# Kernel optimization log

Measured on AMD Instinct MI355X. Metric: run time of the kernel, lower is better.

## Reference

```python
import jax, jax.numpy as jnp
import numpy as np

B, N, NFEAT, NHID, NOUT, NMLP, NCLASS = 32, 1024, 128, 64, 64, 128, 2
ALPHA = 0.2  # leaky relu slope
NEG = -9e15


def setup_inputs() -> dict:
    key = jax.random.key(0)
    ks = jax.random.split(key, 12)
    x = jax.random.normal(ks[0], (B, N, NFEAT), dtype=jnp.float32)
    x_mask = (jax.random.uniform(ks[1], (B, N)) < 0.9).astype(jnp.float32)
    adj = (jax.random.uniform(ks[2], (B, N, N)) < 0.05).astype(jnp.float32)
    adj = jnp.maximum(adj, jnp.eye(N, dtype=jnp.float32)[None])  # self loops
    s = 0.02
    W0 = jax.random.normal(ks[3], (NFEAT, NHID), dtype=jnp.float32) * s
    a0 = jax.random.normal(ks[4], (2 * NHID, 1), dtype=jnp.float32) * s
    Wout = jax.random.normal(ks[5], (NHID, NOUT), dtype=jnp.float32) * s
    aout = jax.random.normal(ks[6], (2 * NOUT, 1), dtype=jnp.float32) * s
    W1 = jax.random.normal(ks[7], (NOUT, NMLP), dtype=jnp.float32) * s
    b1 = jnp.zeros((NMLP,), dtype=jnp.float32)
    W2 = jax.random.normal(ks[8], (NMLP, NCLASS), dtype=jnp.float32) * s
    b2 = jnp.zeros((NCLASS,), dtype=jnp.float32)
    return {"x": x, "x_mask": x_mask, "adj": adj, "W0": W0, "a0": a0,
            "Wout": Wout, "aout": aout, "W1": W1, "b1": b1, "W2": W2, "b2": b2}


def _gat_layer(h, adj, W, a):
    # h: [B,N,F_in], W: [F_in,F_out], a: [2*F_out,1]
    Wh = jnp.einsum('bnf,fh->bnh', h, W)                 # [B,N,F_out]
    d = W.shape[1]
    f1 = Wh @ a[:d]                                      # [B,N,1]
    f2 = Wh @ a[d:]                                      # [B,N,1]
    e = jax.nn.leaky_relu(f1 + jnp.swapaxes(f2, 1, 2), ALPHA)  # [B,N,N]
    e = jnp.where(adj > 0, e, NEG)
    attn = jax.nn.softmax(e, axis=-1)
    return jnp.einsum('bnm,bmh->bnh', attn, Wh)


def reference(x, x_mask, adj, W0, a0, Wout, aout, W1, b1, W2, b2):
    # Only head 0 reaches out_att in the original (zip truncation); dropout is
    # identity in eval mode.
    h = jax.nn.elu(_gat_layer(x, adj, W0, a0))           # concat=True -> elu
    h = jax.nn.elu(_gat_layer(h, adj, Wout, aout))       # F.elu applied outside
    m = x_mask[..., None]
    g = jnp.sum(h * m, axis=1) / jnp.maximum(jnp.sum(x_mask, axis=1, keepdims=True), 1.0)  # masked mean readout [B,NOUT]
    return jax.nn.relu(g @ W1 + b1) @ W2 + b2            # [B,NCLASS]
```

## Files before the change

kernel.cpp:

```cpp
#include <hip/hip_runtime.h>
#include <math.h>

#define BB 32
#define NN 1024
#define NFEAT 128
#define ALPHA 0.2f
#define MAXD 128

#define WH1_TILE_BLOCKS (BB * NN / 64)
#define BM_BLOCKS (BB * NN / 4)
#define ATTN_BLOCKS (BB * NN / 8)

template<int FIN>
__device__ __forceinline__ void wh_tile_body(
    const int blk, const int tid,
    const float* __restrict__ hin, const float* __restrict__ W,
    const float* __restrict__ a, float* __restrict__ Wh,
    float* __restrict__ f1, float* __restrict__ f2) {
  const int tx = tid & 15;
  const int ty = tid >> 4;
  const int row0 = blk * 64 + ty * 4;

  float4 acc[4];
#pragma unroll
  for (int i = 0; i < 4; ++i) acc[i] = make_float4(0.f, 0.f, 0.f, 0.f);

#pragma unroll 4
  for (int k = 0; k < FIN; k += 4) {
    float4 wv[4];
#pragma unroll
    for (int i = 0; i < 4; ++i)
      wv[i] = *reinterpret_cast<const float4*>(&W[(size_t)(k + i) * 64 + tx * 4]);
#pragma unroll
    for (int i = 0; i < 4; ++i) {
      const float4 xv = *reinterpret_cast<const float4*>(
          &hin[(size_t)(row0 + i) * FIN + k]);
      acc[i].x = fmaf(xv.x, wv[0].x, acc[i].x);
      acc[i].y = fmaf(xv.x, wv[0].y, acc[i].y);
      acc[i].z = fmaf(xv.x, wv[0].z, acc[i].z);
      acc[i].w = fmaf(xv.x, wv[0].w, acc[i].w);
      acc[i].x = fmaf(xv.y, wv[1].x, acc[i].x);
      acc[i].y = fmaf(xv.y, wv[1].y, acc[i].y);
      acc[i].z = fmaf(xv.y, wv[1].z, acc[i].z);
      acc[i].w = fmaf(xv.y, wv[1].w, acc[i].w);
      acc[i].x = fmaf(xv.z, wv[2].x, acc[i].x);
      acc[i].y = fmaf(xv.z, wv[2].y, acc[i].y);
      acc[i].z = fmaf(xv.z, wv[2].z, acc[i].z);
      acc[i].w = fmaf(xv.z, wv[2].w, acc[i].w);
      acc[i].x = fmaf(xv.w, wv[3].x, acc[i].x);
      acc[i].y = fmaf(xv.w, wv[3].y, acc[i].y);
      acc[i].z = fmaf(xv.w, wv[3].z, acc[i].z);
      acc[i].w = fmaf(xv.w, wv[3].w, acc[i].w);
    }
  }

  const float4 av1 = *reinterpret_cast<const float4*>(&a[tx * 4]);
  const float4 av2 = *reinterpret_cast<const float4*>(&a[64 + tx * 4]);
#pragma unroll
  for (int i = 0; i < 4; ++i) {
    const int row = row0 + i;
    *reinterpret_cast<float4*>(&Wh[(size_t)row * 64 + tx * 4]) = acc[i];
    float c1 = acc[i].x * av1.x + acc[i].y * av1.y + acc[i].z * av1.z + acc[i].w * av1.w;
    float c2 = acc[i].x * av2.x + acc[i].y * av2.y + acc[i].z * av2.z + acc[i].w * av2.w;
#pragma unroll
    for (int off = 8; off > 0; off >>= 1) {
      c1 += __shfl_xor(c1, off, 64);
      c2 += __shfl_xor(c2, off, 64);
    }
    if (tx == 0) { f1[row] = c1; f2[row] = c2; }
  }
}

__global__ __launch_bounds__(256) void wh1_kernel(
    const float* __restrict__ x, const float* __restrict__ W0,
    const float* __restrict__ a0, float* __restrict__ Wh,
    float* __restrict__ f1, float* __restrict__ f2) {
  wh_tile_body<NFEAT>(blockIdx.x, threadIdx.x, x, W0, a0, Wh, f1, f2);
}

__global__ __launch_bounds__(256) void bitmask_kernel(
    const float* __restrict__ adj, unsigned short* __restrict__ bm) {
  const int wv = threadIdx.x >> 6, lane = threadIdx.x & 63;
  const int row = blockIdx.x * 4 + wv;
  const float* ar = adj + (size_t)row * NN + lane * 16;
  const float4 a0 = *reinterpret_cast<const float4*>(ar);
  const float4 a1 = *reinterpret_cast<const float4*>(ar + 4);
  const float4 a2 = *reinterpret_cast<const float4*>(ar + 8);
  const float4 a3 = *reinterpret_cast<const float4*>(ar + 12);
  unsigned m = 0;
  m |= (a0.x > 0.f ? 1u : 0u);        m |= (a0.y > 0.f ? 2u : 0u);
  m |= (a0.z > 0.f ? 4u : 0u);        m |= (a0.w > 0.f ? 8u : 0u);
  m |= (a1.x > 0.f ? 16u : 0u);       m |= (a1.y > 0.f ? 32u : 0u);
  m |= (a1.z > 0.f ? 64u : 0u);       m |= (a1.w > 0.f ? 128u : 0u);
  m |= (a2.x > 0.f ? 256u : 0u);      m |= (a2.y > 0.f ? 512u : 0u);
  m |= (a2.z > 0.f ? 1024u : 0u);     m |= (a2.w > 0.f ? 2048u : 0u);
  m |= (a3.x > 0.f ? 4096u : 0u);     m |= (a3.y > 0.f ? 8192u : 0u);
  m |= (a3.z > 0.f ? 16384u : 0u);    m |= (a3.w > 0.f ? 32768u : 0u);
  bm[(size_t)row * 64 + lane] = (unsigned short)m;
}

__device__ __forceinline__ int bit_compact(
    const unsigned short* __restrict__ bmrow, unsigned short* msh,
    const int lane) {
  unsigned w = bmrow[lane];
  const int myc = __popc(w);
  int pre = myc;
#pragma unroll
  for (int off = 1; off < 64; off <<= 1) {
    const int v = __shfl_up(pre, off, 64);
    if (lane >= off) pre += v;
  }
  const int total = __shfl(pre, 63, 64);
  int base = pre - myc;
  while (w) {
    const int b = __ffs(w) - 1;
    if (base < MAXD) msh[base] = (unsigned short)(lane * 16 + b);
    w &= w - 1;
    ++base;
  }
  return total < MAXD ? total : MAXD;
}

__device__ __forceinline__ void gather4(
    const float* ps0, const unsigned short* ms0,
    const float* ps1, const unsigned short* ms1,
    const int bound, const float* __restrict__ Whb,
    const int slot, const int fq, float4& outA, float4& outB) {
  float4 accA = make_float4(0.f, 0.f, 0.f, 0.f);
  float4 accB = make_float4(0.f, 0.f, 0.f, 0.f);
  const float* WhF = Whb + fq * 4;
  for (int k = 0; k < bound; k += 4) {
    const int ia = ms0[k + slot];
    const int ib = ms1[k + slot];
    const float pa = ps0[k + slot];
    const float pb = ps1[k + slot];
    const float4 wa = *reinterpret_cast<const float4*>(&WhF[(size_t)ia * 64]);
    const float4 wb = *reinterpret_cast<const float4*>(&WhF[(size_t)ib * 64]);
    accA.x = fmaf(pa, wa.x, accA.x);
    accA.y = fmaf(pa, wa.y, accA.y);
    accA.z = fmaf(pa, wa.z, accA.z);
    accA.w = fmaf(pa, wa.w, accA.w);
    accB.x = fmaf(pb, wb.x, accB.x);
    accB.y = fmaf(pb, wb.y, accB.y);
    accB.z = fmaf(pb, wb.z, accB.z);
    accB.w = fmaf(pb, wb.w, accB.w);
  }
#pragma unroll
  for (int off = 16; off <= 32; off <<= 1) {
    accA.x += __shfl_xor(accA.x, off, 64);
    accA.y += __shfl_xor(accA.y, off, 64);
    accA.z += __shfl_xor(accA.z, off, 64);
    accA.w += __shfl_xor(accA.w, off, 64);
    accB.x += __shfl_xor(accB.x, off, 64);
    accB.y += __shfl_xor(accB.y, off, 64);
    accB.z += __shfl_xor(accB.z, off, 64);
    accB.w += __shfl_xor(accB.w, off, 64);
  }
  outA = accA;
  outB = accB;
}

__device__ __forceinline__ float4 elu4(const float4 v) {
  return make_float4(v.x > 0.f ? v.x : expm1f(v.x),
                     v.y > 0.f ? v.y : expm1f(v.y),
                     v.z > 0.f ? v.z : expm1f(v.z),
                     v.w > 0.f ? v.w : expm1f(v.w));
}

__global__ __launch_bounds__(256) void attn1_kernel(
    const unsigned short* __restrict__ bm,
    const float* __restrict__ f1, const float* __restrict__ f2,
    const float* __restrict__ Wh,
    const float* __restrict__ Wnext, const float* __restrict__ anext,
    float* __restrict__ WhOut, float* __restrict__ f1o,
    float* __restrict__ f2o) {
  __shared__ __align__(16) float ps[4][2][MAXD];
  __shared__ __align__(16) unsigned short msh[4][2][MAXD];
  __shared__ __align__(16) float h1s[4][2][64];
  const int wv = threadIdx.x >> 6, lane = threadIdx.x & 63;
  const int slot = lane >> 4, fq = lane & 15;
  const int j = blockIdx.x;
  const int batch = (j & 7) + 8 * (j >> 10);
  const int cp = (j >> 3) & 127;
  const int row0 = (batch * 256 + 2 * cp) * 4 + wv;

  msh[wv][0][lane] = 0;  msh[wv][0][64 + lane] = 0;
  msh[wv][1][lane] = 0;  msh[wv][1][64 + lane] = 0;
  const int count0 = bit_compact(bm + (size_t)row0 * 64, msh[wv][0], lane);
  const int count1 = bit_compact(bm + (size_t)(row0 + 4) * 64, msh[wv][1], lane);

  const float f1v0 = f1[row0];
  const float f1v1 = f1[row0 + 4];
  const float* f2b = f2 + (size_t)batch * NN;
#pragma unroll
  for (int rr = 0; rr < 2; ++rr) {
    const int cntr = rr == 0 ? count0 : count1;
    const float f1n = rr == 0 ? f1v0 : f1v1;
    const int m0 = msh[wv][rr][lane];
    const int m1 = msh[wv][rr][64 + lane];
    const bool on0 = lane < cntr, on1 = 64 + lane < cntr;
    const float v0 = f1n + f2b[m0];
    const float v1 = f1n + f2b[m1];
    float e0v = on0 ? (v0 > 0.f ? v0 : ALPHA * v0) : -3e38f;
    float e1v = on1 ? (v1 > 0.f ? v1 : ALPHA * v1) : -3e38f;
    float lmax = fmaxf(e0v, e1v);
#pragma unroll
    for (int off = 32; off > 0; off >>= 1) lmax = fmaxf(lmax, __shfl_xor(lmax, off, 64));
    const float p0 = on0 ? __expf(e0v - lmax) : 0.f;
    const float p1 = on1 ? __expf(e1v - lmax) : 0.f;
    float ls = p0 + p1;
#pragma unroll
    for (int off = 32; off > 0; off >>= 1) ls += __shfl_xor(ls, off, 64);
    const float inv = 1.f / ls;
    ps[wv][rr][lane] = p0 * inv;
    ps[wv][rr][64 + lane] = p1 * inv;
  }

  const int cmax = count0 > count1 ? count0 : count1;
  const int bound = (cmax + 3) & ~3;
  const float* Whb = Wh + (size_t)batch * (NN * 64);
  float4 accA, accB;
  gather4(ps[wv][0], msh[wv][0], ps[wv][1], msh[wv][1], bound, Whb,
          slot, fq, accA, accB);
  if (slot == 0) {
    *reinterpret_cast<float4*>(&h1s[wv][0][fq * 4]) = elu4(accA);
    *reinterpret_cast<float4*>(&h1s[wv][1][fq * 4]) = elu4(accB);
  }

  float s0 = 0.f, s1 = 0.f;
#pragma unroll 8
  for (int f = 0; f < 64; ++f) {
    const float w = Wnext[f * 64 + lane];
    s0 = fmaf(h1s[wv][0][f], w, s0);
    s1 = fmaf(h1s[wv][1][f], w, s1);
  }
  WhOut[(size_t)row0 * 64 + lane] = s0;
  WhOut[(size_t)(row0 + 4) * 64 + lane] = s1;
  const float a1v = anext[lane], a2v = anext[64 + lane];
  float c10 = s0 * a1v, c20 = s0 * a2v;
  float c11 = s1 * a1v, c21 = s1 * a2v;
#pragma unroll
  for (int off = 32; off > 0; off >>= 1) {
    c10 += __shfl_xor(c10, off, 64);
    c20 += __shfl_xor(c20, off, 64);
    c11 += __shfl_xor(c11, off, 64);
    c21 += __shfl_xor(c21, off, 64);
  }
  if (lane == 0) {
    f1o[row0] = c10;  f2o[row0] = c20;
    f1o[row0 + 4] = c11;  f2o[row0 + 4] = c21;
  }
}

__global__ __launch_bounds__(256) void attn2_kernel(
    const unsigned short* __restrict__ bm,
    const float* __restrict__ f1, const float* __restrict__ f2,
    const float* __restrict__ Wh, const float* __restrict__ mask,
    float* __restrict__ part2) {
  __shared__ __align__(16) float ps[4][2][MAXD];
  __shared__ __align__(16) unsigned short msh[4][2][MAXD];
  __shared__ __align__(16) float agg[4][2][64];
  const int wv = threadIdx.x >> 6, lane = threadIdx.x & 63;
  const int slot = lane >> 4, fq = lane & 15;
  const int j = blockIdx.x;
  const int batch = (j & 7) + 8 * (j >> 10);
  const int cp = (j >> 3) & 127;
  const int row0 = (batch * 256 + 2 * cp) * 4 + wv;

  msh[wv][0][lane] = 0;  msh[wv][0][64 + lane] = 0;
  msh[wv][1][lane] = 0;  msh[wv][1][64 + lane] = 0;
  const int count0 = bit_compact(bm + (size_t)row0 * 64, msh[wv][0], lane);
  const int count1 = bit_compact(bm + (size_t)(row0 + 4) * 64, msh[wv][1], lane);

  const float* f2b = f2 + (size_t)batch * NN;
  const float f1v[2] = { f1[row0], f1[row0 + 4] };
#pragma unroll
  for (int rr = 0; rr < 2; ++rr) {
    const int cntr = rr == 0 ? count0 : count1;
    const int m0 = msh[wv][rr][lane];
    const int m1 = msh[wv][rr][64 + lane];
    const bool on0 = lane < cntr, on1 = 64 + lane < cntr;
    const float v0 = f1v[rr] + f2b[m0];
    const float v1 = f1v[rr] + f2b[m1];
    float e0v = on0 ? (v0 > 0.f ? v0 : ALPHA * v0) : -3e38f;
    float e1v = on1 ? (v1 > 0.f ? v1 : ALPHA * v1) : -3e38f;
    float lmax = fmaxf(e0v, e1v);
#pragma unroll
    for (int off = 32; off > 0; off >>= 1) lmax = fmaxf(lmax, __shfl_xor(lmax, off, 64));
    const float p0 = on0 ? __expf(e0v - lmax) : 0.f;
    const float p1 = on1 ? __expf(e1v - lmax) : 0.f;
    float ls = p0 + p1;
#pragma unroll
    for (int off = 32; off > 0; off >>= 1) ls += __shfl_xor(ls, off, 64);
    const float inv = 1.f / ls;
    ps[wv][rr][lane] = p0 * inv;
    ps[wv][rr][64 + lane] = p1 * inv;
  }

  const int cmax = count0 > count1 ? count0 : count1;
  const int bound = (cmax + 3) & ~3;
  const float* Whb = Wh + (size_t)batch * (NN * 64);
  float4 accA, accB;
  gather4(ps[wv][0], msh[wv][0], ps[wv][1], msh[wv][1], bound, Whb,
          slot, fq, accA, accB);
  const float mv0 = mask[row0];
  const float mv1 = mask[row0 + 4];
  if (slot == 0) {
    const float4 h0 = elu4(accA);
    const float4 h1 = elu4(accB);
    *reinterpret_cast<float4*>(&agg[wv][0][fq * 4]) =
        make_float4(mv0 * h0.x, mv0 * h0.y, mv0 * h0.z, mv0 * h0.w);
    *reinterpret_cast<float4*>(&agg[wv][1][fq * 4]) =
        make_float4(mv1 * h1.x, mv1 * h1.y, mv1 * h1.z, mv1 * h1.w);
  }
  __syncthreads();
  if (wv < 2)
    part2[((size_t)batch * 256 + 2 * cp + wv) * 64 + lane] =
        (agg[0][wv][lane] + agg[1][wv][lane]) +
        (agg[2][wv][lane] + agg[3][wv][lane]);
}

__global__ __launch_bounds__(256) void mlp2_kernel(
    const float* __restrict__ part2, const float* __restrict__ mask,
    const float* __restrict__ W1, const float* __restrict__ b1,
    const float* __restrict__ W2, const float* __restrict__ b2,
    float* __restrict__ outp) {
  const int b = blockIdx.x;
  const int tid = threadIdx.x;
  const int wv = tid >> 6, lane = tid & 63;
  __shared__ float aggG[4][64];
  __shared__ float msW[4];
  __shared__ float g[64];
  __shared__ float hid[128];

  const float4 mv4 = *reinterpret_cast<const float4*>(&mask[(size_t)b * NN + tid * 4]);
  float ms = (mv4.x + mv4.y) + (mv4.z + mv4.w);
#pragma unroll
  for (int off = 32; off > 0; off >>= 1) ms += __shfl_xor(ms, off, 64);
  if (lane == 0) msW[wv] = ms;

  float gs = 0.f;
  const float* pb = part2 + ((size_t)b * 256 + wv * 64) * 64 + lane;
#pragma unroll 8
  for (int i = 0; i < 64; ++i) gs += pb[(size_t)i * 64];
  aggG[wv][lane] = gs;
  __syncthreads();
  const float denom = fmaxf((msW[0] + msW[1]) + (msW[2] + msW[3]), 1.0f);
  if (tid < 64)
    g[tid] = ((aggG[0][tid] + aggG[1][tid]) + (aggG[2][tid] + aggG[3][tid])) / denom;
  __syncthreads();
  if (tid < 128) {
    float s = b1[tid];
#pragma unroll 8
    for (int k = 0; k < 64; ++k) s += g[k] * W1[k * 128 + tid];
    hid[tid] = fmaxf(s, 0.f);
  }
  __syncthreads();
  if (tid < 2) {
    float o = b2[tid];
    for (int jj = 0; jj < 128; ++jj) o += hid[jj] * W2[jj * 2 + tid];
    outp[b * 2 + tid] = o;
  }
}

extern "C" void kernel_launch(void* const* d_in, const int* in_sizes, int n_in,
                              void* d_out, int out_size, void* d_ws, size_t ws_size,
                              hipStream_t stream) {
  const float* x      = (const float*)d_in[0];
  const float* x_mask = (const float*)d_in[1];
  const float* adj    = (const float*)d_in[2];
  const float* W0     = (const float*)d_in[3];
  const float* a0     = (const float*)d_in[4];
  const float* Wout   = (const float*)d_in[5];
  const float* aout   = (const float*)d_in[6];
  const float* W1     = (const float*)d_in[7];
  const float* b1     = (const float*)d_in[8];
  const float* W2     = (const float*)d_in[9];
  const float* b2     = (const float*)d_in[10];
  float* out = (float*)d_out;

  const int rows = BB * NN;

  float* ws = (float*)d_ws;
  float* Wh  = ws;
  float* Wh2 = Wh + (size_t)rows * 64;
  float* f1  = Wh2 + (size_t)rows * 64;
  float* f2  = f1 + rows;
  float* f1b = f2 + rows;
  float* f2b = f1b + rows;
  unsigned short* bm = (unsigned short*)(f2b + rows);
  float* part2 = (float*)(bm + (size_t)rows * 64);

  bitmask_kernel<<<BM_BLOCKS, 256, 0, stream>>>(adj, bm);
  wh1_kernel<<<WH1_TILE_BLOCKS, 256, 0, stream>>>(x, W0, a0, Wh, f1, f2);
  attn1_kernel<<<ATTN_BLOCKS, 256, 0, stream>>>(
      bm, f1, f2, Wh, Wout, aout, Wh2, f1b, f2b);
  attn2_kernel<<<ATTN_BLOCKS, 256, 0, stream>>>(
      bm, f1b, f2b, Wh2, x_mask, part2);
  mlp2_kernel<<<BB, 256, 0, stream>>>(part2, x_mask, W1, b1, W2, b2, out);
}
```

Baseline: 113.1 us.

## Process four adjacency rows per wave with inline-asm software-pipelined loads

The bitmask kernel now runs 2048 blocks, and each wave handles four rows strided by 8192 instead of one. Loads use inline-asm global_load_dwordx4 with hand-placed s_waitcnt vmcnt counts, so the next row's loads are in flight while the previous row is packed and stored. This is meant to raise memory-level parallelism in what is a pure streaming read of the 128 MB adjacency matrix. In exchange, the hand waitcnt counts are fragile because compiler-emitted stores also count against vmcnt, and the grid shrinks fourfold.

```diff
diff --git a/kernel.cpp b/kernel.cpp
--- a/kernel.cpp
+++ b/kernel.cpp
@@ -6,10 +6,15 @@
 #define NFEAT 128
 #define ALPHA 0.2f
 #define MAXD 128
+#define ROWS (BB * NN)
 
 #define WH1_TILE_BLOCKS (BB * NN / 64)
-#define BM_BLOCKS (BB * NN / 4)
+#define BM_BLOCKS 2048
 #define ATTN_BLOCKS (BB * NN / 8)
+
+__device__ __forceinline__ void gld_f4(float4& d, const float* a) {
+  asm volatile("global_load_dwordx4 %0, %1, off" : "=v"(d) : "v"(a));
+}
 
 template<int FIN>
 __device__ __forceinline__ void wh_tile_body(
@@ -78,25 +83,51 @@
   wh_tile_body<NFEAT>(blockIdx.x, threadIdx.x, x, W0, a0, Wh, f1, f2);
 }
 
+__device__ __forceinline__ unsigned pack16(
+    const float4& a, const float4& b, const float4& c, const float4& d) {
+  unsigned m = 0;
+  m |= (a.x > 0.f ? 1u : 0u);      m |= (a.y > 0.f ? 2u : 0u);
+  m |= (a.z > 0.f ? 4u : 0u);      m |= (a.w > 0.f ? 8u : 0u);
+  m |= (b.x > 0.f ? 16u : 0u);     m |= (b.y > 0.f ? 32u : 0u);
+  m |= (b.z > 0.f ? 64u : 0u);     m |= (b.w > 0.f ? 128u : 0u);
+  m |= (c.x > 0.f ? 256u : 0u);    m |= (c.y > 0.f ? 512u : 0u);
+  m |= (c.z > 0.f ? 1024u : 0u);   m |= (c.w > 0.f ? 2048u : 0u);
+  m |= (d.x > 0.f ? 4096u : 0u);   m |= (d.y > 0.f ? 8192u : 0u);
+  m |= (d.z > 0.f ? 16384u : 0u);  m |= (d.w > 0.f ? 32768u : 0u);
+  return m;
+}
+
 __global__ __launch_bounds__(256) void bitmask_kernel(
     const float* __restrict__ adj, unsigned short* __restrict__ bm) {
-  const int wv = threadIdx.x >> 6, lane = threadIdx.x & 63;
-  const int row = blockIdx.x * 4 + wv;
-  const float* ar = adj + (size_t)row * NN + lane * 16;
-  const float4 a0 = *reinterpret_cast<const float4*>(ar);
-  const float4 a1 = *reinterpret_cast<const float4*>(ar + 4);
-  const float4 a2 = *reinterpret_cast<const float4*>(ar + 8);
-  const float4 a3 = *reinterpret_cast<const float4*>(ar + 12);
-  unsigned m = 0;
-  m |= (a0.x > 0.f ? 1u : 0u);        m |= (a0.y > 0.f ? 2u : 0u);
-  m |= (a0.z > 0.f ? 4u : 0u);        m |= (a0.w > 0.f ? 8u : 0u);
-  m |= (a1.x > 0.f ? 16u : 0u);       m |= (a1.y > 0.f ? 32u : 0u);
-  m |= (a1.z > 0.f ? 64u : 0u);       m |= (a1.w > 0.f ? 128u : 0u);
-  m |= (a2.x > 0.f ? 256u : 0u);      m |= (a2.y > 0.f ? 512u : 0u);
-  m |= (a2.z > 0.f ? 1024u : 0u);     m |= (a2.w > 0.f ? 2048u : 0u);
-  m |= (a3.x > 0.f ? 4096u : 0u);     m |= (a3.y > 0.f ? 8192u : 0u);
-  m |= (a3.z > 0.f ? 16384u : 0u);    m |= (a3.w > 0.f ? 32768u : 0u);
-  bm[(size_t)row * 64 + lane] = (unsigned short)m;
+  const int wid = blockIdx.x * 4 + (threadIdx.x >> 6);
+  const int lane = threadIdx.x & 63;
+  const int r0 = wid, r1 = wid + 8192, r2 = wid + 16384, r3 = wid + 24576;
+  const float* p0 = adj + (size_t)r0 * NN + lane * 16;
+  const float* p1 = adj + (size_t)r1 * NN + lane * 16;
+  const float* p2 = adj + (size_t)r2 * NN + lane * 16;
+  const float* p3 = adj + (size_t)r3 * NN + lane * 16;
+  float4 A0, A1, A2, A3, B0, B1, B2, B3;
+
+  gld_f4(A0, p0);      gld_f4(A1, p0 + 4);
+  gld_f4(A2, p0 + 8);  gld_f4(A3, p0 + 12);
+  gld_f4(B0, p1);      gld_f4(B1, p1 + 4);
+  gld_f4(B2, p1 + 8);  gld_f4(B3, p1 + 12);
+  asm volatile("s_waitcnt vmcnt(4)" ::: "memory");
+  __builtin_amdgcn_sched_barrier(0);
+  bm[(size_t)r0 * 64 + lane] = (unsigned short)pack16(A0, A1, A2, A3);
+  gld_f4(A0, p2);      gld_f4(A1, p2 + 4);
+  gld_f4(A2, p2 + 8);  gld_f4(A3, p2 + 12);
+  asm volatile("s_waitcnt vmcnt(5)" ::: "memory");
+  __builtin_amdgcn_sched_barrier(0);
+  bm[(size_t)r1 * 64 + lane] = (unsigned short)pack16(B0, B1, B2, B3);
+  gld_f4(B0, p3);      gld_f4(B1, p3 + 4);
+  gld_f4(B2, p3 + 8);  gld_f4(B3, p3 + 12);
+  asm volatile("s_waitcnt vmcnt(5)" ::: "memory");
+  __builtin_amdgcn_sched_barrier(0);
+  bm[(size_t)r2 * 64 + lane] = (unsigned short)pack16(A0, A1, A2, A3);
+  asm volatile("s_waitcnt vmcnt(1)" ::: "memory");
+  __builtin_amdgcn_sched_barrier(0);
+  bm[(size_t)r3 * 64 + lane] = (unsigned short)pack16(B0, B1, B2, B3);
 }
 
 __device__ __forceinline__ int bit_compact(
@@ -379,7 +410,7 @@
   const float* b2     = (const float*)d_in[10];
   float* out = (float*)d_out;
 
-  const int rows = BB * NN;
+  const int rows = ROWS;
 
   float* ws = (float*)d_ws;
   float* Wh  = ws;
```

After: 113.0 us. About the same (-0.1%).
